# Kernel optimization log

Hardware: AMD Instinct MI355X
Metric: run time of the kernel (lower is better)

Reference implementation:

```python
import jax, jax.numpy as jnp
import numpy as np

B, S, D = 1, 2048, 4096
H, KVH, DH = 32, 8, 128
NEG_INF = jnp.finfo(jnp.float32).min


def rotate_half(x):
    x1, x2 = jnp.split(x, 2, axis=-1)
    return jnp.concatenate([-x2, x1], axis=-1)


def setup_inputs() -> dict:
    key = jax.random.key(0)
    ks = jax.random.split(key, 6)
    hidden_states = jax.random.normal(ks[0], (B, S, D), dtype=jnp.float32)
    # proper llama RoPE tables
    inv_freq = 1.0 / (10000.0 ** (jnp.arange(0, DH, 2, dtype=jnp.float32) / DH))
    pos = jnp.arange(S, dtype=jnp.float32)
    freqs = pos[:, None] * inv_freq[None, :]            # [S, DH/2]
    emb = jnp.concatenate([freqs, freqs], axis=-1)       # [S, DH]
    cos = jnp.cos(emb)
    sin = jnp.sin(emb)
    # additive causal mask [B,1,S,S]
    causal = jnp.tril(jnp.ones((S, S), dtype=bool))
    attention_mask = jnp.where(causal, 0.0, NEG_INF)[None, None].astype(jnp.float32)
    sc = 0.02
    Wq = jax.random.normal(ks[1], (D, H * DH), dtype=jnp.float32) * sc
    Wk = jax.random.normal(ks[2], (D, KVH * DH), dtype=jnp.float32) * sc
    Wv = jax.random.normal(ks[3], (D, KVH * DH), dtype=jnp.float32) * sc
    Wo = jax.random.normal(ks[4], (H * DH, D), dtype=jnp.float32) * sc
    return {"hidden_states": hidden_states, "cos": cos, "sin": sin,
            "attention_mask": attention_mask, "Wq": Wq, "Wk": Wk, "Wv": Wv, "Wo": Wo}


def reference(hidden_states, cos, sin, attention_mask, Wq, Wk, Wv, Wo):
    b, s, _ = hidden_states.shape
    scaling = DH ** -0.5
    q = (hidden_states @ Wq).reshape(b, s, H, DH).transpose(0, 2, 1, 3)     # [B,H,S,DH]
    k = (hidden_states @ Wk).reshape(b, s, KVH, DH).transpose(0, 2, 1, 3)   # [B,KVH,S,DH]
    v = (hidden_states @ Wv).reshape(b, s, KVH, DH).transpose(0, 2, 1, 3)
    c = cos[None, None]  # [1,1,S,DH]
    sn = sin[None, None]
    q = q * c + rotate_half(q) * sn
    k = k * c + rotate_half(k) * sn
    n_rep = H // KVH
    k = jnp.repeat(k, n_rep, axis=1)  # [B,H,S,DH]
    v = jnp.repeat(v, n_rep, axis=1)
    scores = jnp.einsum('bhqd,bhkd->bhqk', q, k) * scaling
    scores = jnp.maximum(scores + attention_mask, NEG_INF)
    probs = jax.nn.softmax(scores.astype(jnp.float32), axis=-1).astype(q.dtype)
    attn = jnp.einsum('bhqk,bhkd->bhqd', probs, v)
    attn = attn.transpose(0, 2, 1, 3).reshape(b, s, H * DH)
    return attn @ Wo
```

## Files before the change

kernel.cpp:

```cpp
#include <hip/hip_runtime.h>
#include <hip/hip_bf16.h>
#include <stdint.h>

typedef unsigned short u16;
typedef unsigned int u32;
typedef __bf16 bf16x8 __attribute__((ext_vector_type(8)));
typedef float f32x4 __attribute__((ext_vector_type(4)));
typedef float f32x16 __attribute__((ext_vector_type(16)));
typedef u16 u16x8 __attribute__((ext_vector_type(8)));

#define S_LEN 2048
#define DMODEL 4096
#define NHEADS 32
#define NKVH 8
#define DHEAD 128
#define LDQK 6144

__device__ __forceinline__ float bf2f(u16 x) {
    union { u32 i; float f; } u; u.i = ((u32)x) << 16; return u.f;
}
__device__ __forceinline__ u16 f2bf(float f) {
    union { float f; u32 i; } u; u.f = f;
    u32 x = u.i;
    return (u16)((x + 0x7fffu + ((x >> 16) & 1u)) >> 16);
}
__device__ __forceinline__ bf16x8 ld_bf8(const void* p) {
    int4 v = *(const int4*)p;
    return __builtin_bit_cast(bf16x8, v);
}

__global__ void k_cvt(const float* __restrict__ in, u16* __restrict__ out, int n8) {
    int i = blockIdx.x * 256 + threadIdx.x;
    if (i >= n8) return;
    const float4* p = (const float4*)in + (size_t)i * 2;
    float4 a = p[0], b = p[1];
    u16x8 o;
    o[0]=f2bf(a.x); o[1]=f2bf(a.y); o[2]=f2bf(a.z); o[3]=f2bf(a.w);
    o[4]=f2bf(b.x); o[5]=f2bf(b.y); o[6]=f2bf(b.z); o[7]=f2bf(b.w);
    *((u16x8*)out + i) = o;
}

__global__ __launch_bounds__(256)
void k_transpose_w(const float* __restrict__ in, u16* __restrict__ out, int R, int C) {
    __shared__ u16 tile[64][68];
    const int c0 = blockIdx.x * 64, r0 = blockIdx.y * 64;
    const int tid = threadIdx.x, lane = tid & 63, wid = tid >> 6;

    const int ch = lane & 15;
    const int rr = (lane >> 4) + wid * 4;
    #pragma unroll
    for (int it = 0; it < 4; it++) {
        int r = rr + it * 16;
        float4 v = *(const float4*)(in + (size_t)(r0 + r) * C + c0 + ch * 4);
        u16* t = &tile[r][ch * 4];
        t[0] = f2bf(v.x); t[1] = f2bf(v.y); t[2] = f2bf(v.z); t[3] = f2bf(v.w);
    }
    __syncthreads();
    const int k8 = lane & 7;
    const int cb = (lane >> 3) + wid * 8;
    #pragma unroll
    for (int it = 0; it < 2; it++) {
        int c = cb + it * 32;
        u16x8 o;
        #pragma unroll
        for (int i = 0; i < 8; i++) o[i] = tile[k8 * 8 + i][c];
        *(u16x8*)(out + (size_t)(c0 + c) * R + r0 + k8 * 8) = o;
    }
}

template<typename TIN>
__global__ void k_transpose_bf16(const TIN* __restrict__ in, u16* __restrict__ out,
                                 int R, int C, int ldin) {
    __shared__ u16 tile[32][33];
    int c0 = blockIdx.x * 32, r0 = blockIdx.y * 32;
    int tx = threadIdx.x & 31, ty = threadIdx.x >> 5;
    #pragma unroll
    for (int i = 0; i < 4; i++) {
        int r = ty + i * 8;
        TIN v = in[(size_t)(r0 + r) * ldin + c0 + tx];
        if constexpr (sizeof(TIN) == 4) tile[r][tx] = f2bf((float)v);
        else tile[r][tx] = (u16)v;
    }
    __syncthreads();
    #pragma unroll
    for (int i = 0; i < 4; i++) {
        int r = ty + i * 8;
        out[(size_t)(c0 + r) * R + r0 + tx] = tile[tx][r];
    }
}

__global__ void k_rope(u16* __restrict__ X, const float* __restrict__ cosT,
                       const float* __restrict__ sinT, int nh, int ld) {
    int idx = blockIdx.x * 256 + threadIdx.x;
    int d = idx & 63;
    int h = (idx >> 6) % nh;
    int s = idx / (64 * nh);
    u16* p = X + (size_t)s * ld + h * DHEAD;
    float x1 = bf2f(p[d]), x2 = bf2f(p[d + 64]);
    float c1 = cosT[s * DHEAD + d],      s1 = sinT[s * DHEAD + d];
    float c2 = cosT[s * DHEAD + d + 64], s2 = sinT[s * DHEAD + d + 64];
    p[d]      = f2bf(x1 * c1 - x2 * s1);
    p[d + 64] = f2bf(x2 * c2 + x1 * s2);
}

typedef const __attribute__((address_space(1))) u32 GBUF;
typedef __attribute__((address_space(3))) u32 LBUF;

template<typename OUT_T>
__global__ __launch_bounds__(256)
void k_gemm_bt2(const u16* __restrict__ A, const u16* __restrict__ Bt,
                OUT_T* __restrict__ C, int M, int N, int K) {
    __shared__ __align__(16) u16 As[128 * 64];
    __shared__ __align__(16) u16 Bs[128 * 64];
    const int m0 = blockIdx.y * 128, n0 = blockIdx.x * 128;
    const int tid = threadIdx.x, lane = tid & 63, wid = tid >> 6;
    const int wr = wid >> 1, wc = wid & 1;
    const int g = lane >> 4, lr = lane & 15;

    const u16* sA[4]; const u16* sB[4]; u32 dste[4];
    #pragma unroll
    for (int j = 0; j < 4; j++) {
        int c = j * 256 + tid;
        int row = c >> 3;
        int colsw = (c & 7) ^ (row & 7);
        sA[j] = A  + (size_t)(m0 + row) * K + colsw * 8;
        sB[j] = Bt + (size_t)(n0 + row) * K + colsw * 8;
        dste[j] = (u32)c * 8;
    }
    auto rdoff = [&](int row, int kk) -> u32 {
        return (u32)(row * 128 + ((((kk << 2) + g) ^ (row & 7)) << 4));
    };

    f32x4 acc[4][4] = {};

    for (int k0 = 0; k0 < K; k0 += 64) {
        __syncthreads();
        #pragma unroll
        for (int j = 0; j < 4; j++)
            __builtin_amdgcn_global_load_lds((GBUF*)(sA[j] + k0), (LBUF*)(As + dste[j]), 16, 0, 0);
        #pragma unroll
        for (int j = 0; j < 4; j++)
            __builtin_amdgcn_global_load_lds((GBUF*)(sB[j] + k0), (LBUF*)(Bs + dste[j]), 16, 0, 0);
        __syncthreads();

        bf16x8 af[4][2], bfv[4][2];
        #pragma unroll
        for (int i = 0; i < 4; i++)
            #pragma unroll
            for (int kk = 0; kk < 2; kk++)
                af[i][kk] = ld_bf8((const char*)As + rdoff(wr * 64 + i * 16 + lr, kk));
        #pragma unroll
        for (int n = 0; n < 4; n++)
            #pragma unroll
            for (int kk = 0; kk < 2; kk++)
                bfv[n][kk] = ld_bf8((const char*)Bs + rdoff(wc * 64 + n * 16 + lr, kk));
        #pragma unroll
        for (int i = 0; i < 4; i++)
            #pragma unroll
            for (int n = 0; n < 4; n++)
                #pragma unroll
                for (int kk = 0; kk < 2; kk++)
                    acc[i][n] = __builtin_amdgcn_mfma_f32_16x16x32_bf16(
                        af[i][kk], bfv[n][kk], acc[i][n], 0, 0, 0);
    }
    #pragma unroll
    for (int i = 0; i < 4; i++)
        #pragma unroll
        for (int n = 0; n < 4; n++)
            #pragma unroll
            for (int r = 0; r < 4; r++) {
                int row = m0 + wr * 64 + i * 16 + g * 4 + r;
                int col = n0 + wc * 64 + n * 16 + lr;
                float v = acc[i][n][r];
                if constexpr (sizeof(OUT_T) == 2) C[(size_t)row * N + col] = f2bf(v);
                else                              C[(size_t)row * N + col] = v;
            }
}

__global__ __launch_bounds__(256, 2)
void k_attn3(const u16* __restrict__ Qb, const u16* __restrict__ Kb,
             const u16* __restrict__ VbT, u16* __restrict__ Ab) {
    extern __shared__ __align__(16) char smem[];

    const int bid = blockIdx.x;
    const int idx = bid & 255;
    int t = idx & 7; if (bid >> 8) t = 15 - t;
    const int h = idx >> 3, hk = h >> 2;
    const int tid = threadIdx.x, lane = tid & 63, wid = tid >> 6;
    const int ql = lane & 31, hi = lane >> 5;
    const float scale = 0.08838834764831845f;
    const int NIT = 2 * t + 2;
    const int q0w = 128 * t + 32 * wid;
    const int qg = q0w + ql;

    const int krow_l = lane >> 4, kc16 = lane & 15;
    const int vrow_l = lane >> 3, vc8  = lane & 7;

    auto stage = [&](int buf, int k0) {
        u16* KsD = (u16*)smem + buf * 8192;
        u16* VtD = (u16*)(smem + 32768) + buf * 8192;
        #pragma unroll
        for (int j = 0; j < 4; j++) {
            int rowt = wid * 16 + j * 4 + krow_l;
            int c16  = kc16 ^ (rowt & 7);
            __builtin_amdgcn_global_load_lds(
                (GBUF*)(Kb + (size_t)(k0 + rowt) * LDQK + hk * DHEAD + c16 * 8),
                (LBUF*)(KsD + (wid * 16 + j * 4) * 128), 16, 0, 0);
        }
        #pragma unroll
        for (int j = 0; j < 4; j++) {
            int rowt = wid * 32 + j * 8 + vrow_l;
            int c8   = vc8 ^ (rowt & 7);
            __builtin_amdgcn_global_load_lds(
                (GBUF*)(VbT + (size_t)(hk * DHEAD + rowt) * S_LEN + k0 + c8 * 8),
                (LBUF*)(VtD + (wid * 32 + j * 8) * 64), 16, 0, 0);
        }
    };

    bf16x8 qf[8];
    {
        const u16* qrow = Qb + (size_t)qg * LDQK + h * DHEAD;
        #pragma unroll
        for (int dc = 0; dc < 8; dc++)
            qf[dc] = ld_bf8(qrow + dc * 16 + hi * 8);
    }

    f32x16 acc[4] = {};
    float m = -1e30f, lsum = 0.f;
    const int imax = 2 * t + (wid >> 1);

    stage(0, 0);
    asm volatile("s_waitcnt vmcnt(0)" ::: "memory");
    __builtin_amdgcn_s_barrier();

    for (int i = 0; i < NIT; i++) {
        if (i + 1 < NIT) stage((i + 1) & 1, (i + 1) * 64);

        if (i <= imax) {
            const char* KsB = smem + (i & 1) * 16384;
            const char* VtB = smem + 32768 + (i & 1) * 16384;

            f32x16 s0 = {}, s1 = {};
            __builtin_amdgcn_s_setprio(1);
            #pragma unroll
            for (int dc = 0; dc < 8; dc++) {
                int r0 = ql, r1 = 32 + ql;
                bf16x8 kf0 = ld_bf8(KsB + r0 * 256 + (((2 * dc + hi) ^ (r0 & 7)) << 4));
                bf16x8 kf1 = ld_bf8(KsB + r1 * 256 + (((2 * dc + hi) ^ (r1 & 7)) << 4));
                s0 = __builtin_amdgcn_mfma_f32_32x32x16_bf16(kf0, qf[dc], s0, 0, 0, 0);
                s1 = __builtin_amdgcn_mfma_f32_32x32x16_bf16(kf1, qf[dc], s1, 0, 0, 0);
            }
            __builtin_amdgcn_s_setprio(0);

            bool diag = (64 * i + 63 > q0w);
            #pragma unroll
            for (int r = 0; r < 16; r++) {
                int kloc = (r & 3) + 8 * (r >> 2) + 4 * hi;
                float v0 = s0[r] * scale, v1 = s1[r] * scale;
                if (diag) {
                    int kg = 64 * i + kloc;
                    if (kg > qg) v0 = -1e30f;
                    if (kg + 32 > qg) v1 = -1e30f;
                }
                s0[r] = v0; s1[r] = v1;
            }

            float t8[8];
            #pragma unroll
            for (int z = 0; z < 8; z++)
                t8[z] = fmaxf(fmaxf(s0[2 * z], s0[2 * z + 1]),
                              fmaxf(s1[2 * z], s1[2 * z + 1]));
            float mx = fmaxf(fmaxf(fmaxf(t8[0], t8[1]), fmaxf(t8[2], t8[3])),
                             fmaxf(fmaxf(t8[4], t8[5]), fmaxf(t8[6], t8[7])));
            mx = fmaxf(mx, __shfl_xor(mx, 32, 64));
            bool sk = (mx <= m + 8.0f);
            float mn = sk ? m : mx;
            float corr = sk ? 1.0f : __expf(m - mn);
            m = mn;

            float ts0 = 0.f, ts1 = 0.f, ts2 = 0.f, ts3 = 0.f;
            #pragma unroll
            for (int z = 0; z < 8; z++) {
                s0[z]     = __expf(s0[z]     - mn); ts0 += s0[z];
                s0[z + 8] = __expf(s0[z + 8] - mn); ts1 += s0[z + 8];
                s1[z]     = __expf(s1[z]     - mn); ts2 += s1[z];
                s1[z + 8] = __expf(s1[z + 8] - mn); ts3 += s1[z + 8];
            }
            float ts = (ts0 + ts1) + (ts2 + ts3);
            ts += __shfl_xor(ts, 32, 64);
            lsum = lsum * corr + ts;
            if (!__all(sk)) {
                #pragma unroll
                for (int r = 0; r < 16; r++) {
                    float c = __shfl(corr, (r & 3) + 8 * (r >> 2) + 4 * hi, 64);
                    acc[0][r] *= c; acc[1][r] *= c; acc[2][r] *= c; acc[3][r] *= c;
                }
            }

            bf16x8 pf[4];
            #pragma unroll
            for (int g2 = 0; g2 < 2; g2++)
                #pragma unroll
                for (int ksl = 0; ksl < 2; ksl++) {
                    u32 ua0, ua1, ua2, ua3;
                    {
                        float a0 = g2 ? s1[8 * ksl + 0] : s0[8 * ksl + 0];
                        float a1 = g2 ? s1[8 * ksl + 1] : s0[8 * ksl + 1];
                        float a2 = g2 ? s1[8 * ksl + 2] : s0[8 * ksl + 2];
                        float a3 = g2 ? s1[8 * ksl + 3] : s0[8 * ksl + 3];
                        float a4 = g2 ? s1[8 * ksl + 4] : s0[8 * ksl + 4];
                        float a5 = g2 ? s1[8 * ksl + 5] : s0[8 * ksl + 5];
                        float a6 = g2 ? s1[8 * ksl + 6] : s0[8 * ksl + 6];
                        float a7 = g2 ? s1[8 * ksl + 7] : s0[8 * ksl + 7];
                        asm("v_cvt_pk_bf16_f32 %0, %1, %2" : "=v"(ua0) : "v"(a0), "v"(a1));
                        asm("v_cvt_pk_bf16_f32 %0, %1, %2" : "=v"(ua1) : "v"(a2), "v"(a3));
                        asm("v_cvt_pk_bf16_f32 %0, %1, %2" : "=v"(ua2) : "v"(a4), "v"(a5));
                        asm("v_cvt_pk_bf16_f32 %0, %1, %2" : "=v"(ua3) : "v"(a6), "v"(a7));
                    }
                    u32 sa0 = __shfl_xor(ua0, 32, 64), sa1 = __shfl_xor(ua1, 32, 64);
                    u32 sa2 = __shfl_xor(ua2, 32, 64), sa3 = __shfl_xor(ua3, 32, 64);
                    int4 w4 = hi ? make_int4(sa2, sa3, ua2, ua3)
                                 : make_int4(ua0, ua1, sa0, sa1);
                    pf[2 * g2 + ksl] = __builtin_bit_cast(bf16x8, w4);
                }

            __builtin_amdgcn_s_setprio(1);
            #pragma unroll
            for (int db = 0; db < 4; db++) {
                int row = 32 * db + ql;
                #pragma unroll
                for (int ks = 0; ks < 4; ks++) {
                    bf16x8 vf = ld_bf8(VtB + row * 128 + (((2 * ks + hi) ^ (row & 7)) << 4));
                    acc[db] = __builtin_amdgcn_mfma_f32_32x32x16_bf16(pf[ks], vf, acc[db], 0, 0, 0);
                }
            }
            __builtin_amdgcn_s_setprio(0);
        }

        asm volatile("s_waitcnt lgkmcnt(0)" ::: "memory");
        __builtin_amdgcn_sched_barrier(0);
        asm volatile("s_waitcnt vmcnt(0)" ::: "memory");
        __builtin_amdgcn_s_barrier();
    }

    #pragma unroll
    for (int r = 0; r < 16; r++) {
        int crow = (r & 3) + 8 * (r >> 2) + 4 * hi;
        float riv = 1.0f / __shfl(lsum, crow, 64);
        #pragma unroll
        for (int db = 0; db < 4; db++)
            Ab[(size_t)(q0w + crow) * DMODEL + h * DHEAD + db * 32 + ql]
                = f2bf(acc[db][r] * riv);
    }
}

extern "C" void kernel_launch(void* const* d_in, const int* in_sizes, int n_in,
                              void* d_out, int out_size, void* d_ws, size_t ws_size,
                              hipStream_t stream) {
    const float* hidden = (const float*)d_in[0];
    const float* cosT   = (const float*)d_in[1];
    const float* sinT   = (const float*)d_in[2];
    const float* Wq = (const float*)d_in[4];
    const float* Wk = (const float*)d_in[5];
    const float* Wv = (const float*)d_in[6];
    const float* Wo = (const float*)d_in[7];
    float* out = (float*)d_out;
    char* ws = (char*)d_ws;

    u16* Xbf   = (u16*)ws;
    u16* WqkvT = (u16*)(ws + (16u << 20));
    u16* VbT   = (u16*)(ws + (16u << 20));
    u16* WoT   = (u16*)(ws + (64u << 20));
    u16* QKVb  = (u16*)(ws + (96u << 20));
    u16* Ab    = Xbf;

    k_cvt<<<dim3((S_LEN * DMODEL / 8) / 256), 256, 0, stream>>>(hidden, Xbf, S_LEN * DMODEL / 8);
    k_transpose_w<<<dim3(4096 / 64, 4096 / 64), 256, 0, stream>>>(Wq, WqkvT, 4096, 4096);
    k_transpose_w<<<dim3(1024 / 64, 4096 / 64), 256, 0, stream>>>(Wk, WqkvT + (size_t)4096 * 4096, 4096, 1024);
    k_transpose_w<<<dim3(1024 / 64, 4096 / 64), 256, 0, stream>>>(Wv, WqkvT + (size_t)5120 * 4096, 4096, 1024);
    k_transpose_w<<<dim3(4096 / 64, 4096 / 64), 256, 0, stream>>>(Wo, WoT, 4096, 4096);

    k_gemm_bt2<u16><<<dim3(6144 / 128, 2048 / 128), 256, 0, stream>>>(Xbf, WqkvT, QKVb, 2048, 6144, 4096);

    k_rope<<<(2048 * 32 * 64) / 256, 256, 0, stream>>>(QKVb, cosT, sinT, 32, LDQK);
    k_rope<<<(2048 * 8 * 64) / 256, 256, 0, stream>>>(QKVb + 4096, cosT, sinT, 8, LDQK);

    k_transpose_bf16<u16><<<dim3(1024 / 32, 2048 / 32), 256, 0, stream>>>(QKVb + 5120, VbT, 2048, 1024, LDQK);

    hipFuncSetAttribute((const void*)k_attn3, hipFuncAttributeMaxDynamicSharedMemorySize, 65536);
    k_attn3<<<dim3(512), 256, 65536, stream>>>(QKVb, QKVb + 4096, VbT, Ab);

    k_gemm_bt2<float><<<dim3(4096 / 128, 2048 / 128), 256, 0, stream>>>(Ab, WoT, out, 2048, 4096, 4096);
}
```

Before: 359.4 us.

## Triple-buffer K/V tiles in attention and reorder blocks longest-first

```diff
diff --git a/kernel.cpp b/kernel.cpp
--- a/kernel.cpp
+++ b/kernel.cpp
@@ -177,15 +177,14 @@
             }
 }
 
-__global__ __launch_bounds__(256, 2)
+__global__ __launch_bounds__(256, 1)
 void k_attn3(const u16* __restrict__ Qb, const u16* __restrict__ Kb,
              const u16* __restrict__ VbT, u16* __restrict__ Ab) {
     extern __shared__ __align__(16) char smem[];
 
     const int bid = blockIdx.x;
-    const int idx = bid & 255;
-    int t = idx & 7; if (bid >> 8) t = 15 - t;
-    const int h = idx >> 3, hk = h >> 2;
+    const int t = 15 - (bid >> 5);
+    const int h = bid & 31, hk = h >> 2;
     const int tid = threadIdx.x, lane = tid & 63, wid = tid >> 6;
     const int ql = lane & 31, hi = lane >> 5;
     const float scale = 0.08838834764831845f;
@@ -197,8 +196,8 @@
     const int vrow_l = lane >> 3, vc8  = lane & 7;
 
     auto stage = [&](int buf, int k0) {
-        u16* KsD = (u16*)smem + buf * 8192;
-        u16* VtD = (u16*)(smem + 32768) + buf * 8192;
+        u16* KsD = (u16*)(smem + buf * 16384);
+        u16* VtD = (u16*)(smem + 49152 + buf * 16384);
         #pragma unroll
         for (int j = 0; j < 4; j++) {
             int rowt = wid * 16 + j * 4 + krow_l;
@@ -230,15 +229,20 @@
     const int imax = 2 * t + (wid >> 1);
 
     stage(0, 0);
-    asm volatile("s_waitcnt vmcnt(0)" ::: "memory");
+    if (NIT > 1) stage(1, 64);
+    __builtin_amdgcn_sched_barrier(0);
+    if (NIT > 1) { asm volatile("s_waitcnt vmcnt(8)" ::: "memory"); }
+    else         { asm volatile("s_waitcnt vmcnt(0)" ::: "memory"); }
+    __builtin_amdgcn_sched_barrier(0);
     __builtin_amdgcn_s_barrier();
 
+    int bcur = 0, bst = 2;
     for (int i = 0; i < NIT; i++) {
-        if (i + 1 < NIT) stage((i + 1) & 1, (i + 1) * 64);
+        if (i + 2 < NIT) stage(bst, (i + 2) * 64);
 
         if (i <= imax) {
-            const char* KsB = smem + (i & 1) * 16384;
-            const char* VtB = smem + 32768 + (i & 1) * 16384;
+            const char* KsB = smem + bcur * 16384;
+            const char* VtB = smem + 49152 + bcur * 16384;
 
             f32x16 s0 = {}, s1 = {};
             __builtin_amdgcn_s_setprio(1);
@@ -337,10 +341,16 @@
             __builtin_amdgcn_s_setprio(0);
         }
 
-        asm volatile("s_waitcnt lgkmcnt(0)" ::: "memory");
-        __builtin_amdgcn_sched_barrier(0);
-        asm volatile("s_waitcnt vmcnt(0)" ::: "memory");
-        __builtin_amdgcn_s_barrier();
+        if (i + 1 < NIT) {
+            asm volatile("s_waitcnt lgkmcnt(0)" ::: "memory");
+            __builtin_amdgcn_sched_barrier(0);
+            if (i + 2 < NIT) { asm volatile("s_waitcnt vmcnt(8)" ::: "memory"); }
+            else             { asm volatile("s_waitcnt vmcnt(0)" ::: "memory"); }
+            __builtin_amdgcn_sched_barrier(0);
+            __builtin_amdgcn_s_barrier();
+        }
+        bcur = (bcur == 2) ? 0 : bcur + 1;
+        bst  = (bst  == 2) ? 0 : bst  + 1;
     }
 
     #pragma unroll
@@ -387,8 +397,8 @@
 
     k_transpose_bf16<u16><<<dim3(1024 / 32, 2048 / 32), 256, 0, stream>>>(QKVb + 5120, VbT, 2048, 1024, LDQK);
 
-    hipFuncSetAttribute((const void*)k_attn3, hipFuncAttributeMaxDynamicSharedMemorySize, 65536);
-    k_attn3<<<dim3(512), 256, 65536, stream>>>(QKVb, QKVb + 4096, VbT, Ab);
+    hipFuncSetAttribute((const void*)k_attn3, hipFuncAttributeMaxDynamicSharedMemorySize, 98304);
+    k_attn3<<<dim3(512), 256, 98304, stream>>>(QKVb, QKVb + 4096, VbT, Ab);
 
     k_gemm_bt2<float><<<dim3(4096 / 128, 2048 / 128), 256, 0, stream>>>(Ab, WoT, out, 2048, 4096, 4096);
 }
```

After: 371.6 us. 3.4% more time.
